# Kernel optimization log

Hardware: AMD Instinct MI355X
Metric: run time of the kernel (lower is better)

Reference implementation:

```python
import jax, jax.numpy as jnp
import numpy as np
from jax import lax

H = 512
V = 32000
B = 64
S = 64
T = 32
TQ = 32
NUM_HOP = 3


def _p(key, shape, scale=0.05):
    return jax.random.normal(key, shape, dtype=jnp.float32) * scale


def setup_inputs() -> dict:
    key = jax.random.key(0)
    ks = jax.random.split(key, 20)
    inp = {}
    inp["contexts"] = jax.random.randint(ks[0], (B, S, T), 0, V)
    inp["questions"] = jax.random.randint(ks[1], (B, TQ), 0, V)
    inp["emb"] = _p(ks[2], (V, H), 1.0)
    # input module: bidirectional GRU (torch gate order r,z,n)
    inp["Wih_f"] = _p(ks[3], (3 * H, H)); inp["Whh_f"] = _p(ks[4], (3 * H, H))
    inp["bih_f"] = jnp.zeros((3 * H,), jnp.float32); inp["bhh_f"] = jnp.zeros((3 * H,), jnp.float32)
    inp["Wih_b"] = _p(ks[5], (3 * H, H)); inp["Whh_b"] = _p(ks[6], (3 * H, H))
    inp["bih_b"] = jnp.zeros((3 * H,), jnp.float32); inp["bhh_b"] = jnp.zeros((3 * H,), jnp.float32)
    # question module GRU
    inp["qWih"] = _p(ks[7], (3 * H, H)); inp["qWhh"] = _p(ks[8], (3 * H, H))
    inp["qbih"] = jnp.zeros((3 * H,), jnp.float32); inp["qbhh"] = jnp.zeros((3 * H,), jnp.float32)
    # attention GRU cell (note: source reuses br as both biases)
    inp["Wr"] = _p(ks[9], (H, H)); inp["Ur"] = _p(ks[10], (H, H)); inp["br"] = jnp.ones((H,), jnp.float32)
    inp["W"] = _p(ks[11], (H, H)); inp["U"] = _p(ks[12], (H, H))
    # episodic memory gate MLP + next-memory projection
    inp["z1_w"] = _p(ks[13], (H, 4 * H)); inp["z1_b"] = jnp.zeros((H,), jnp.float32)
    inp["z2_w"] = _p(ks[14], (1, H)); inp["z2_b"] = jnp.zeros((1,), jnp.float32)
    inp["nm_w"] = _p(ks[15], (H, 3 * H)); inp["nm_b"] = jnp.zeros((H,), jnp.float32)
    # answer module
    inp["ans_w"] = _p(ks[16], (V, 2 * H)); inp["ans_b"] = jnp.zeros((V,), jnp.float32)
    return inp


def _pos_enc(slen, elen):
    # l[s, e] = 1 - s/slen - (e/elen)*(1 - 2*s/slen); indexed by SENTENCE dim, as in source
    s = np.arange(slen, dtype=np.float64)[:, None]
    e = np.arange(elen, dtype=np.float64)[None, :]
    l = 1.0 - s / slen - (e / elen) * (1.0 - 2.0 * s / slen)
    return jnp.asarray(l, dtype=jnp.float32)  # (S, H)


def _gru(x, Wih, Whh, bih, bhh, reverse=False):
    # x: (B, T, H); torch nn.GRU math with gate order r, z, n
    Bn, Tn, Hn = x.shape
    h0 = jnp.zeros((Bn, Hn), x.dtype)

    def step(h, xt):
        gx = xt @ Wih.T + bih
        gh = h @ Whh.T + bhh
        xr, xz, xn = jnp.split(gx, 3, axis=-1)
        hr, hz, hn = jnp.split(gh, 3, axis=-1)
        r = jax.nn.sigmoid(xr + hr)
        z = jax.nn.sigmoid(xz + hz)
        n = jnp.tanh(xn + r * hn)
        h_new = (1.0 - z) * n + z * h
        return h_new, h_new

    h_last, hs = lax.scan(step, h0, jnp.swapaxes(x, 0, 1), reverse=reverse)
    return jnp.swapaxes(hs, 0, 1), h_last


def _dmn(emb, Wih_f, Whh_f, bih_f, bhh_f, Wih_b, Whh_b, bih_b, bhh_b,
         qWih, qWhh, qbih, qbhh, Wr, Ur, br, W, U,
         z1_w, z1_b, z2_w, z2_b, nm_w, nm_b, ans_w, ans_b,
         contexts, questions):
    emb0 = emb.at[0].set(0.0)  # padding_idx=0
    Bn, Sn, Tn = contexts.shape
    Hn = emb.shape[1]
    # ---- input module ----
    ce = emb0[contexts]                                   # (B,S,T,H)
    pe = _pos_enc(Sn, Hn)                                 # (S,H), broadcast over tokens (faithful)
    facts_in = jnp.sum(ce * pe[None, :, None, :], axis=2)  # (B,S,H)
    hf, _ = _gru(facts_in, Wih_f, Whh_f, bih_f, bhh_f, reverse=False)
    hb, _ = _gru(facts_in, Wih_b, Whh_b, bih_b, bhh_b, reverse=True)
    facts = hf + hb                                       # (B,S,H); dropout = identity (eval)
    # ---- question module ----
    _, q = _gru(emb0[questions], qWih, qWhh, qbih, qbhh)  # (B,H)
    # ---- episodic memory hops ----
    facts_t = jnp.swapaxes(facts, 0, 1)                   # (S,B,H)
    M = q
    for _ in range(NUM_HOP):
        qb = q[:, None, :]
        Mb = M[:, None, :]
        z = jnp.concatenate([facts * qb, facts * Mb,
                             jnp.abs(facts - qb), jnp.abs(facts - Mb)], axis=-1)  # (B,S,4H)
        g1 = jnp.tanh(z @ z1_w.T + z1_b)
        G = jax.nn.softmax((g1 @ z2_w.T + z2_b)[..., 0], axis=1)  # (B,S)

        def agru(c, sg):
            fact, g = sg
            r = jax.nn.sigmoid(fact @ Wr + c @ Ur + br)
            ht = jnp.tanh(fact @ W + r * (c @ U) + br)  # source reuses br as b
            return g[:, None] * ht + (1.0 - g[:, None]) * c, None

        C, _ = lax.scan(agru, jnp.zeros((Bn, Hn), facts.dtype), (facts_t, G.T))
        M = jax.nn.relu(jnp.concatenate([M, C, q], axis=-1) @ nm_w.T + nm_b)
    # ---- answer module (dropout = identity) ----
    preds = jnp.concatenate([M, q], axis=-1) @ ans_w.T + ans_b  # (B,V)
    return preds


def reference(contexts, questions, emb, Wih_f, Whh_f, bih_f, bhh_f,
              Wih_b, Whh_b, bih_b, bhh_b, qWih, qWhh, qbih, qbhh,
              Wr, Ur, br, W, U, z1_w, z1_b, z2_w, z2_b, nm_w, nm_b,
              ans_w, ans_b):
    return _dmn(emb, Wih_f, Whh_f, bih_f, bhh_f, Wih_b, Whh_b, bih_b, bhh_b,
                qWih, qWhh, qbih, qbhh, Wr, Ur, br, W, U,
                z1_w, z1_b, z2_w, z2_b, nm_w, nm_b, ans_w, ans_b,
                contexts, questions)
```

## Files before the change

### kernel.cpp

```cpp
#include <hip/hip_runtime.h>
#include <cstddef>
#include <cstdint>

namespace {

constexpr int H  = 512;
constexpr int V  = 32000;
constexpr int B  = 64;
constexpr int S  = 64;
constexpr int T  = 32;
constexpr int TQ = 32;

typedef unsigned short ushort_t;
typedef __attribute__((ext_vector_type(8))) short bf16x8;
typedef __attribute__((ext_vector_type(4))) short bf16x4;
typedef __attribute__((ext_vector_type(4))) float f32x4;
typedef __attribute__((ext_vector_type(4))) unsigned u32x4;

__device__ __forceinline__ ushort_t f2bf(float f) {
  union { float f; unsigned u; } v; v.f = f;
  return (ushort_t)((v.u + 0x7FFFu + ((v.u >> 16) & 1u)) >> 16);
}

__device__ __forceinline__ float sigm(float x) { return 1.f / (1.f + expf(-x)); }

__device__ __forceinline__ bf16x8 pack8(f32x4 a, f32x4 b) {
  bf16x8 r;
  r[0] = (short)f2bf(a[0]); r[1] = (short)f2bf(a[1]);
  r[2] = (short)f2bf(a[2]); r[3] = (short)f2bf(a[3]);
  r[4] = (short)f2bf(b[0]); r[5] = (short)f2bf(b[1]);
  r[6] = (short)f2bf(b[2]); r[7] = (short)f2bf(b[3]);
  return r;
}

__device__ __forceinline__ u32x4 load16c(const void* p) {
  u32x4 v;
  asm volatile("global_load_dwordx4 %0, %1, off sc0 sc1" : "=v"(v) : "v"(p));
  return v;
}
__device__ __forceinline__ void store2c(ushort_t* p, unsigned v) {
  asm volatile("global_store_short %0, %1, off sc0 sc1" :: "v"(p), "v"(v) : "memory");
}
__device__ __forceinline__ void store1cu(unsigned* p, unsigned v) {
  asm volatile("global_store_dword %0, %1, off sc0 sc1" :: "v"(p), "v"(v) : "memory");
}
__device__ __forceinline__ void waitvm0() {
  asm volatile("s_waitcnt vmcnt(0)" ::: "memory");
  __builtin_amdgcn_sched_barrier(0);
}

__device__ __forceinline__ void flag_barrier(unsigned* flags, int rank,
                                             unsigned step1, int t, int lane, int wv) {
  waitvm0();
  __syncthreads();
  if (t == 0) store1cu(flags + rank * 32, step1);
  if (wv == 0) {
    const unsigned* fp = flags + (lane & 7) * 32;
    for (;;) {
      unsigned v;
      asm volatile("global_load_dword %0, %1, off sc0 sc1" : "=v"(v) : "v"(fp));
      asm volatile("s_waitcnt vmcnt(0)" ::: "memory");
      const int ok = (lane >= 8) || (v >= step1);
      if (__all(ok)) break;
      __builtin_amdgcn_s_sleep(1);
    }
  }
  __syncthreads();
}

__global__ __launch_bounds__(256) void k_embed_facts(const int* __restrict__ ctx,
                                                     const float* __restrict__ emb,
                                                     float* __restrict__ facts_in) {
  const int bs = blockIdx.x;
  const int s  = bs & (S - 1);
  const int t  = threadIdx.x;
  __shared__ int sidx[T];
  if (t < T) sidx[t] = ctx[(size_t)bs * T + t];
  __syncthreads();
  float a0 = 0.f, a1 = 0.f;
  for (int tt = 0; tt < T; ++tt) {
    const int ix = sidx[tt];
    if (ix != 0) {
      const float* e = emb + ((size_t)ix << 9);
      a0 += e[t];
      a1 += e[t + 256];
    }
  }
  const float sf = (float)s * (1.f / 64.f);
  const float c1 = 1.f - sf;
  const float c2 = (1.f - 2.f * sf) * (1.f / 512.f);
  facts_in[((size_t)bs << 9) + t]       = a0 * (c1 - (float)t * c2);
  facts_in[((size_t)bs << 9) + t + 256] = a1 * (c1 - (float)(t + 256) * c2);
}

__global__ __launch_bounds__(256) void k_embed_q(const int* __restrict__ qidx,
                                                 const float* __restrict__ emb,
                                                 float* __restrict__ qe) {
  const int bt = blockIdx.x;
  const int t  = threadIdx.x;
  const int ix = qidx[bt];
  float v0 = 0.f, v1 = 0.f;
  if (ix != 0) {
    const float* e = emb + ((size_t)ix << 9);
    v0 = e[t];
    v1 = e[t + 256];
  }
  qe[((size_t)bt << 9) + t]       = v0;
  qe[((size_t)bt << 9) + t + 256] = v1;
}

__global__ __launch_bounds__(256) void k_transpose512(const float* __restrict__ src,
                                                      float* __restrict__ dst) {
  __shared__ float tile[32][33];
  const int x0 = blockIdx.x * 32, y0 = blockIdx.y * 32;
  for (int i = threadIdx.y; i < 32; i += 8)
    tile[i][threadIdx.x] = src[(size_t)(y0 + i) * H + x0 + threadIdx.x];
  __syncthreads();
  for (int i = threadIdx.y; i < 32; i += 8)
    dst[(size_t)(x0 + i) * H + y0 + threadIdx.x] = tile[threadIdx.x][i];
}

template <bool A_BF16, int ACT>
__global__ __launch_bounds__(256) void k_gemm_mfma(const void* __restrict__ Av,
                                                   const float* __restrict__ Bm,
                                                   const float* __restrict__ bias,
                                                   float* __restrict__ C,
                                                   int M, int N, int K) {
  __shared__ __align__(16) ushort_t As[64][72];
  __shared__ __align__(16) ushort_t Bs[64][72];
  const int t    = threadIdx.x;
  const int lane = t & 63;
  const int w    = t >> 6;
  const int wr   = w >> 1, wc = w & 1;
  const int m0 = blockIdx.y << 6, n0 = blockIdx.x << 6;
  const int row = t >> 2;
  const int ch  = t & 3;

  f32x4 acc[2][2] = {};

  for (int k0 = 0; k0 < K; k0 += 64) {
    if (A_BF16) {
      const ushort_t* A16 = (const ushort_t*)Av;
#pragma unroll
      for (int cc = 0; cc < 2; ++cc) {
        const int c8 = ch + cc * 4;
        const uint4 v = *(const uint4*)(A16 + (size_t)(m0 + row) * K + k0 + c8 * 8);
        *(uint4*)&As[row][c8 * 8] = v;
      }
    } else {
      const float* Af = (const float*)Av;
#pragma unroll
      for (int cc = 0; cc < 2; ++cc) {
        const int c8 = ch + cc * 4;
        const float* src = Af + (size_t)(m0 + row) * K + k0 + c8 * 8;
        *(bf16x8*)&As[row][c8 * 8] = pack8(*(const f32x4*)src, *(const f32x4*)(src + 4));
      }
    }
#pragma unroll
    for (int cc = 0; cc < 2; ++cc) {
      const int c8 = ch + cc * 4;
      const float* srb = Bm + (size_t)(n0 + row) * K + k0 + c8 * 8;
      *(bf16x8*)&Bs[row][c8 * 8] = pack8(*(const f32x4*)srb, *(const f32x4*)(srb + 4));
    }
    __syncthreads();
#pragma unroll
    for (int ks = 0; ks < 2; ++ks) {
      bf16x8 a[2], b[2];
#pragma unroll
      for (int fr = 0; fr < 2; ++fr)
        a[fr] = *(const bf16x8*)&As[wr * 32 + fr * 16 + (lane & 15)][ks * 32 + (lane >> 4) * 8];
#pragma unroll
      for (int fc = 0; fc < 2; ++fc)
        b[fc] = *(const bf16x8*)&Bs[wc * 32 + fc * 16 + (lane & 15)][ks * 32 + (lane >> 4) * 8];
#pragma unroll
      for (int fr = 0; fr < 2; ++fr)
#pragma unroll
        for (int fc = 0; fc < 2; ++fc)
          acc[fr][fc] = __builtin_amdgcn_mfma_f32_16x16x32_bf16(a[fr], b[fc], acc[fr][fc], 0, 0, 0);
    }
    __syncthreads();
  }
#pragma unroll
  for (int fr = 0; fr < 2; ++fr) {
#pragma unroll
    for (int fc = 0; fc < 2; ++fc) {
      const int rbase = m0 + wr * 32 + fr * 16 + ((lane >> 4) << 2);
      const int col   = n0 + wc * 32 + fc * 16 + (lane & 15);
      const float bv  = bias ? bias[col] : 0.f;
#pragma unroll
      for (int j = 0; j < 4; ++j) {
        float v = acc[fr][fc][j] + bv;
        if (ACT == 1) v = tanhf(v);
        if (ACT == 2) v = fmaxf(v, 0.f);
        C[(size_t)(rbase + j) * N + col] = v;
      }
    }
  }
}

__global__ __launch_bounds__(256) void k_build_z16(const float* __restrict__ facts,
                                                   const float* __restrict__ q,
                                                   const float* __restrict__ M,
                                                   ushort_t* __restrict__ z) {
  const int bs = blockIdx.x;
  const int b  = bs >> 6;
  const int t  = threadIdx.x;
  const size_t zb = (size_t)bs << 11;
  for (int c = t; c < 512; c += 256) {
    const float f  = facts[((size_t)bs << 9) + c];
    const float qv = q[(b << 9) + c];
    const float mv = M[(b << 9) + c];
    z[zb + c]        = f2bf(f * qv);
    z[zb + 512 + c]  = f2bf(f * mv);
    z[zb + 1024 + c] = f2bf(fabsf(f - qv));
    z[zb + 1536 + c] = f2bf(fabsf(f - mv));
  }
}

__global__ __launch_bounds__(256) void k_gemm_cat3(const float* __restrict__ Mv,
                                                   const float* __restrict__ Cv,
                                                   const float* __restrict__ qv,
                                                   const float* __restrict__ Bm,
                                                   const float* __restrict__ bias,
                                                   float* __restrict__ C) {
  constexpr int N = 512, K = 1536;
  __shared__ __align__(16) ushort_t As[64][72];
  __shared__ __align__(16) ushort_t Bs[64][72];
  const int t    = threadIdx.x;
  const int lane = t & 63;
  const int w    = t >> 6;
  const int wr   = w >> 1, wc = w & 1;
  const int n0 = blockIdx.x << 6;
  const int row = t >> 2;
  const int ch  = t & 3;

  f32x4 acc[2][2] = {};

  for (int k0 = 0; k0 < K; k0 += 64) {
    const int seg = k0 >> 9;
    const float* src = (seg == 0) ? Mv : (seg == 1) ? Cv : qv;
    const int kb = k0 & 511;
#pragma unroll
    for (int cc = 0; cc < 2; ++cc) {
      const int c8 = ch + cc * 4;
      const float* fp = src + ((size_t)row << 9) + kb + c8 * 8;
      *(bf16x8*)&As[row][c8 * 8] = pack8(*(const f32x4*)fp, *(const f32x4*)(fp + 4));
      const float* srb = Bm + (size_t)(n0 + row) * K + k0 + c8 * 8;
      *(bf16x8*)&Bs[row][c8 * 8] = pack8(*(const f32x4*)srb, *(const f32x4*)(srb + 4));
    }
    __syncthreads();
#pragma unroll
    for (int ks = 0; ks < 2; ++ks) {
      bf16x8 a[2], bb[2];
#pragma unroll
      for (int fr = 0; fr < 2; ++fr)
        a[fr] = *(const bf16x8*)&As[wr * 32 + fr * 16 + (lane & 15)][ks * 32 + (lane >> 4) * 8];
#pragma unroll
      for (int fc = 0; fc < 2; ++fc)
        bb[fc] = *(const bf16x8*)&Bs[wc * 32 + fc * 16 + (lane & 15)][ks * 32 + (lane >> 4) * 8];
#pragma unroll
      for (int fr = 0; fr < 2; ++fr)
#pragma unroll
        for (int fc = 0; fc < 2; ++fc)
          acc[fr][fc] = __builtin_amdgcn_mfma_f32_16x16x32_bf16(a[fr], bb[fc], acc[fr][fc], 0, 0, 0);
    }
    __syncthreads();
  }
#pragma unroll
  for (int fr = 0; fr < 2; ++fr) {
#pragma unroll
    for (int fc = 0; fc < 2; ++fc) {
      const int rbase = wr * 32 + fr * 16 + ((lane >> 4) << 2);
      const int col   = n0 + wc * 32 + fc * 16 + (lane & 15);
      const float bv  = bias[col];
#pragma unroll
      for (int j = 0; j < 4; ++j)
        C[(size_t)(rbase + j) * N + col] = fmaxf(acc[fr][fc][j] + bv, 0.f);
    }
  }
}

__global__ __launch_bounds__(256) void k_gemm_cat2(const float* __restrict__ Mv,
                                                   const float* __restrict__ qv,
                                                   const float* __restrict__ Bm,
                                                   const float* __restrict__ bias,
                                                   float* __restrict__ C) {
  constexpr int N = 32000, K = 1024;
  __shared__ __align__(16) ushort_t As[64][72];
  __shared__ __align__(16) ushort_t Bs[64][72];
  const int t    = threadIdx.x;
  const int lane = t & 63;
  const int w    = t >> 6;
  const int wr   = w >> 1, wc = w & 1;
  const int n0 = blockIdx.x << 6;
  const int row = t >> 2;
  const int ch  = t & 3;

  f32x4 acc[2][2] = {};

  for (int k0 = 0; k0 < K; k0 += 64) {
    const float* src = (k0 < 512) ? Mv : qv;
    const int kb = k0 & 511;
#pragma unroll
    for (int cc = 0; cc < 2; ++cc) {
      const int c8 = ch + cc * 4;
      const float* fp = src + ((size_t)row << 9) + kb + c8 * 8;
      *(bf16x8*)&As[row][c8 * 8] = pack8(*(const f32x4*)fp, *(const f32x4*)(fp + 4));
      const float* srb = Bm + (size_t)(n0 + row) * K + k0 + c8 * 8;
      *(bf16x8*)&Bs[row][c8 * 8] = pack8(*(const f32x4*)srb, *(const f32x4*)(srb + 4));
    }
    __syncthreads();
#pragma unroll
    for (int ks = 0; ks < 2; ++ks) {
      bf16x8 a[2], bb[2];
#pragma unroll
      for (int fr = 0; fr < 2; ++fr)
        a[fr] = *(const bf16x8*)&As[wr * 32 + fr * 16 + (lane & 15)][ks * 32 + (lane >> 4) * 8];
#pragma unroll
      for (int fc = 0; fc < 2; ++fc)
        bb[fc] = *(const bf16x8*)&Bs[wc * 32 + fc * 16 + (lane & 15)][ks * 32 + (lane >> 4) * 8];
#pragma unroll
      for (int fr = 0; fr < 2; ++fr)
#pragma unroll
        for (int fc = 0; fc < 2; ++fc)
          acc[fr][fc] = __builtin_amdgcn_mfma_f32_16x16x32_bf16(a[fr], bb[fc], acc[fr][fc], 0, 0, 0);
    }
    __syncthreads();
  }
#pragma unroll
  for (int fr = 0; fr < 2; ++fr) {
#pragma unroll
    for (int fc = 0; fc < 2; ++fc) {
      const int rbase = wr * 32 + fr * 16 + ((lane >> 4) << 2);
      const int col   = n0 + wc * 32 + fc * 16 + (lane & 15);
      const float bv  = bias[col];
#pragma unroll
      for (int j = 0; j < 4; ++j)
        C[(size_t)(rbase + j) * N + col] = acc[fr][fc][j] + bv;
    }
  }
}

__global__ __launch_bounds__(256, 1) void k_gru_scan_mfma(
    const float* __restrict__ Whh_f, const float* __restrict__ bhh_f,
    const float* __restrict__ Whh_b, const float* __restrict__ bhh_b,
    const float* __restrict__ qWhh,  const float* __restrict__ qbhh,
    const float* __restrict__ gx_f, const float* __restrict__ gx_b,
    const float* __restrict__ gx_q,
    ushort_t* __restrict__ H16, float* __restrict__ qbuf,
    float* __restrict__ facts, float* __restrict__ hb_all,
    unsigned* __restrict__ flags_base) {
  const int bx   = blockIdx.x;
  const int grp  = bx >> 3;
  const int rank = bx & 7;
  const int gru  = grp >> 2;
  const int ib   = grp & 3;

  const float* Whh; const float* bhh; const float* gx;
  float* out_seq; int seqlen, rev;
  if (gru == 0)      { Whh = Whh_f; bhh = bhh_f; gx = gx_f; out_seq = facts;   seqlen = S;  rev = 0; }
  else if (gru == 1) { Whh = Whh_b; bhh = bhh_b; gx = gx_b; out_seq = hb_all;  seqlen = S;  rev = 1; }
  else               { Whh = qWhh;  bhh = qbhh;  gx = gx_q; out_seq = nullptr; seqlen = TQ; rev = 0; }
  ushort_t* Hb0 = H16 + gru * 65536;
  ushort_t* Hb1 = Hb0 + 32768;

  __shared__ __align__(16) ushort_t hl[16 * 520];

  const int t    = threadIdx.x;
  const int lane = t & 63;
  const int wv   = t >> 6;
  const int nt   = (rank << 2) + wv;
  const int lm   = lane & 15;
  const int lk   = lane >> 4;
  const int col  = (nt << 4) + lm;

  bf16x8 wf[3][16];
#pragma unroll
  for (int g = 0; g < 3; ++g) {
    const float* wrow = Whh + ((size_t)(g * 512 + col) << 9) + (lk << 3);
#pragma unroll
    for (int ks = 0; ks < 16; ++ks) {
      const float* p = wrow + ks * 32;
      wf[g][ks] = pack8(*(const f32x4*)p, *(const f32x4*)(p + 4));
    }
  }
  const float bv0 = bhh[col], bv1 = bhh[512 + col], bv2 = bhh[1024 + col];
  unsigned* flags = flags_base + grp * 8 * 32;

  float xr[4], xz[4], xn[4];
  {
    const int xidx = rev ? (seqlen - 1) : 0;
#pragma unroll
    for (int j = 0; j < 4; ++j) {
      const int b = (ib << 4) + (lk << 2) + j;
      const size_t gxrow = ((size_t)b * seqlen + xidx) * 1536;
      xr[j] = gx[gxrow + col];
      xz[j] = gx[gxrow + 512 + col];
      xn[j] = gx[gxrow + 1024 + col];
    }
  }

  float hp[4] = {0.f, 0.f, 0.f, 0.f};

  for (int s = 0; s < seqlen; ++s) {
    if (s == 0) {
      for (int i = t; i < 4160; i += 256) ((unsigned*)hl)[i] = 0u;
    } else {
      const ushort_t* Hp16 = (s & 1) ? Hb1 : Hb0;
      u32x4 v[4];
#pragma unroll
      for (int u = 0; u < 4; ++u) {
        const int i = (u << 8) + t;
        v[u] = load16c(Hp16 + ((size_t)((ib << 4) + (i >> 6)) << 9) + ((i << 3) & 511));
      }
      waitvm0();
#pragma unroll
      for (int u = 0; u < 4; ++u) {
        const int i = (u << 8) + t;
        *(u32x4*)&hl[(i >> 6) * 520 + ((i << 3) & 511)] = v[u];
      }
    }
    __syncthreads();

    f32x4 acc0 = {}, acc1 = {}, acc2 = {};
#pragma unroll
    for (int ks = 0; ks < 16; ++ks) {
      const bf16x8 a = *(const bf16x8*)&hl[lm * 520 + (ks << 5) + (lk << 3)];
      acc0 = __builtin_amdgcn_mfma_f32_16x16x32_bf16(a, wf[0][ks], acc0, 0, 0, 0);
      acc1 = __builtin_amdgcn_mfma_f32_16x16x32_bf16(a, wf[1][ks], acc1, 0, 0, 0);
      acc2 = __builtin_amdgcn_mfma_f32_16x16x32_bf16(a, wf[2][ks], acc2, 0, 0, 0);
    }

    const int xidx = rev ? (seqlen - 1 - s) : s;
    ushort_t* Hn16 = (s & 1) ? Hb0 : Hb1;
#pragma unroll
    for (int j = 0; j < 4; ++j) {
      const int b = (ib << 4) + (lk << 2) + j;
      const float r = sigm(xr[j] + acc0[j] + bv0);
      const float z = sigm(xz[j] + acc1[j] + bv1);
      const float n = tanhf(xn[j] + r * (acc2[j] + bv2));
      const float hnew = (1.f - z) * n + z * hp[j];
      hp[j] = hnew;
      if (s + 1 < seqlen) store2c(Hn16 + ((size_t)b << 9) + col, (unsigned)f2bf(hnew));
      if (out_seq) out_seq[((size_t)(b * S + xidx) << 9) + col] = hnew;
      if (gru == 2 && s == seqlen - 1) qbuf[((size_t)b << 9) + col] = hnew;
    }

    if (s + 1 < seqlen) {
      const int xidx2 = rev ? (seqlen - 2 - s) : (s + 1);
      float nxr[4], nxz[4], nxn[4];
#pragma unroll
      for (int j = 0; j < 4; ++j) {
        const int b = (ib << 4) + (lk << 2) + j;
        const size_t gxrow = ((size_t)b * seqlen + xidx2) * 1536;
        nxr[j] = gx[gxrow + col];
        nxz[j] = gx[gxrow + 512 + col];
        nxn[j] = gx[gxrow + 1024 + col];
      }
      flag_barrier(flags, rank, (unsigned)(s + 1), t, lane, wv);
#pragma unroll
      for (int j = 0; j < 4; ++j) { xr[j] = nxr[j]; xz[j] = nxz[j]; xn[j] = nxn[j]; }
    }
  }
}

__global__ __launch_bounds__(256, 1) void k_agru_scan_mfma(
    const float* __restrict__ UrT, const float* __restrict__ UT,
    const float* __restrict__ fRW, const float* __restrict__ fW,
    const float* __restrict__ br, const float* __restrict__ G,
    ushort_t* __restrict__ C16, float* __restrict__ C0f,
    unsigned* __restrict__ flags_base) {
  const int bx   = blockIdx.x;
  const int grp  = bx >> 3;
  const int rank = bx & 7;
  ushort_t* Cb0 = C16;
  ushort_t* Cb1 = C16 + 32768;

  __shared__ __align__(16) ushort_t cl[16 * 520];

  const int t    = threadIdx.x;
  const int lane = t & 63;
  const int wv   = t >> 6;
  const int nt   = (rank << 2) + wv;
  const int lm   = lane & 15;
  const int lk   = lane >> 4;
  const int col  = (nt << 4) + lm;

  bf16x8 wfr[16], wfu[16];
  {
    const float* r0 = UrT + ((size_t)col << 9) + (lk << 3);
    const float* r1 = UT  + ((size_t)col << 9) + (lk << 3);
#pragma unroll
    for (int ks = 0; ks < 16; ++ks) {
      wfr[ks] = pack8(*(const f32x4*)(r0 + ks * 32), *(const f32x4*)(r0 + ks * 32 + 4));
      wfu[ks] = pack8(*(const f32x4*)(r1 + ks * 32), *(const f32x4*)(r1 + ks * 32 + 4));
    }
  }
  const float brv = br[col];
  unsigned* flags = flags_base + grp * 8 * 32;

  float fr[4], fw[4], gg[4];
#pragma unroll
  for (int j = 0; j < 4; ++j) {
    const int b = (grp << 4) + (lk << 2) + j;
    const size_t fi = ((size_t)(b * S) << 9) + col;
    fr[j] = fRW[fi];
    fw[j] = fW[fi];
    gg[j] = G[b << 6];
  }

  float cp[4] = {0.f, 0.f, 0.f, 0.f};

  for (int s = 0; s < S; ++s) {
    if (s == 0) {
      for (int i = t; i < 4160; i += 256) ((unsigned*)cl)[i] = 0u;
    } else {
      const ushort_t* Cp16 = (s & 1) ? Cb1 : Cb0;
      u32x4 v[4];
#pragma unroll
      for (int u = 0; u < 4; ++u) {
        const int i = (u << 8) + t;
        v[u] = load16c(Cp16 + ((size_t)((grp << 4) + (i >> 6)) << 9) + ((i << 3) & 511));
      }
      waitvm0();
#pragma unroll
      for (int u = 0; u < 4; ++u) {
        const int i = (u << 8) + t;
        *(u32x4*)&cl[(i >> 6) * 520 + ((i << 3) & 511)] = v[u];
      }
    }
    __syncthreads();

    f32x4 accr = {}, accu = {};
#pragma unroll
    for (int ks = 0; ks < 16; ++ks) {
      const bf16x8 a = *(const bf16x8*)&cl[lm * 520 + (ks << 5) + (lk << 3)];
      accr = __builtin_amdgcn_mfma_f32_16x16x32_bf16(a, wfr[ks], accr, 0, 0, 0);
      accu = __builtin_amdgcn_mfma_f32_16x16x32_bf16(a, wfu[ks], accu, 0, 0, 0);
    }

    ushort_t* Cn16 = (s & 1) ? Cb0 : Cb1;
#pragma unroll
    for (int j = 0; j < 4; ++j) {
      const int b = (grp << 4) + (lk << 2) + j;
      const float r  = sigm(fr[j] + accr[j] + brv);
      const float ht = tanhf(fw[j] + r * accu[j] + brv);
      const float cnew = gg[j] * ht + (1.f - gg[j]) * cp[j];
      cp[j] = cnew;
      if (s + 1 < S) store2c(Cn16 + ((size_t)b << 9) + col, (unsigned)f2bf(cnew));
      else           C0f[((size_t)b << 9) + col] = cnew;
    }

    if (s + 1 < S) {
      float nfr[4], nfw[4], ngg[4];
#pragma unroll
      for (int j = 0; j < 4; ++j) {
        const int b = (grp << 4) + (lk << 2) + j;
        const size_t fi = ((size_t)(b * S + s + 1) << 9) + col;
        nfr[j] = fRW[fi];
        nfw[j] = fW[fi];
        ngg[j] = G[(b << 6) + s + 1];
      }
      flag_barrier(flags, rank, (unsigned)(s + 1), t, lane, wv);
#pragma unroll
      for (int j = 0; j < 4; ++j) { fr[j] = nfr[j]; fw[j] = nfw[j]; gg[j] = ngg[j]; }
    }
  }
}

__global__ __launch_bounds__(256) void k_add(float* __restrict__ a, const float* __restrict__ b) {
  const size_t i = (((size_t)blockIdx.x << 8) + threadIdx.x) << 2;
  float4 x = *(float4*)(a + i);
  const float4 y = *(const float4*)(b + i);
  x.x += y.x; x.y += y.y; x.z += y.z; x.w += y.w;
  *(float4*)(a + i) = x;
}

__global__ __launch_bounds__(256) void k_score_softmax(const float* __restrict__ g1,
                                                       const float* __restrict__ z2w,
                                                       const float* __restrict__ z2b,
                                                       float* __restrict__ G) {
  const int b = blockIdx.x, t = threadIdx.x;
  const int wave = t >> 6, lane = t & 63;
  __shared__ float sc[64];
  for (int si = 0; si < 16; ++si) {
    const int s = wave * 16 + si;
    const float* row = g1 + ((size_t)(b * S + s) << 9) + lane * 8;
    const float* w   = z2w + lane * 8;
    float p = 0.f;
#pragma unroll
    for (int k = 0; k < 8; ++k) p += row[k] * w[k];
#pragma unroll
    for (int off = 32; off; off >>= 1) p += __shfl_xor(p, off);
    if (lane == 0) sc[s] = p + z2b[0];
  }
  __syncthreads();
  if (wave == 0) {
    const float v = sc[lane];
    float m = v;
#pragma unroll
    for (int off = 32; off; off >>= 1) m = fmaxf(m, __shfl_xor(m, off));
    const float e = expf(v - m);
    float su = e;
#pragma unroll
    for (int off = 32; off; off >>= 1) su += __shfl_xor(su, off);
    G[(b << 6) + lane] = e / su;
  }
}

}

extern "C" void kernel_launch(void* const* d_in, const int* in_sizes, int n_in,
                              void* d_out, int out_size, void* d_ws, size_t ws_size,
                              hipStream_t stream) {
  const int*   contexts  = (const int*)d_in[0];
  const int*   questions = (const int*)d_in[1];
  const float* emb   = (const float*)d_in[2];
  const float* Wih_f = (const float*)d_in[3];
  const float* Whh_f = (const float*)d_in[4];
  const float* bih_f = (const float*)d_in[5];
  const float* bhh_f = (const float*)d_in[6];
  const float* Wih_b = (const float*)d_in[7];
  const float* Whh_b = (const float*)d_in[8];
  const float* bih_b = (const float*)d_in[9];
  const float* bhh_b = (const float*)d_in[10];
  const float* qWih  = (const float*)d_in[11];
  const float* qWhh  = (const float*)d_in[12];
  const float* qbih  = (const float*)d_in[13];
  const float* qbhh  = (const float*)d_in[14];
  const float* Wr    = (const float*)d_in[15];
  const float* Ur    = (const float*)d_in[16];
  const float* br    = (const float*)d_in[17];
  const float* Wm    = (const float*)d_in[18];
  const float* Um    = (const float*)d_in[19];
  const float* z1_w  = (const float*)d_in[20];
  const float* z1_b  = (const float*)d_in[21];
  const float* z2_w  = (const float*)d_in[22];
  const float* z2_b  = (const float*)d_in[23];
  const float* nm_w  = (const float*)d_in[24];
  const float* nm_b  = (const float*)d_in[25];
  const float* ans_w = (const float*)d_in[26];
  const float* ans_b = (const float*)d_in[27];
  (void)in_sizes; (void)n_in; (void)out_size; (void)ws_size;

  float* ws = (float*)d_ws;
  float* WrT      = ws + 0;
  float* UrT      = ws + 262144;
  float* WT       = ws + 524288;
  float* UT       = ws + 786432;
  float* facts_in = ws + 1048576;
  float* qe       = ws + 3145728;
  float* gx_f     = ws + 4194304;
  float* gx_b     = ws + 10485760;
  float* gx_q     = ws + 16777216;
  float* facts    = ws + 19922944;
  float* hb       = ws + 22020096;
  float* Hbuf     = ws + 24117248;
  float* C0       = ws + 24313856;
  float* M0       = ws + 24379392;
  float* M1       = ws + 24412160;
  float* Mq       = ws + 24543232;
  float* Gm       = ws + 24608768;
  ushort_t* H16 = (ushort_t*)Hbuf;
  float* qbuf   = Hbuf + 98304;
  ushort_t* C16 = (ushort_t*)(Hbuf + 131072);
  ushort_t* zb16 = (ushort_t*)gx_f;
  float* g1  = gx_q;
  float* fRW = facts_in;
  float* fW  = hb;
  float* preds = (float*)d_out;
  unsigned* bar = (unsigned*)Mq;
  float* q = qbuf;

  hipMemsetAsync(bar, 0, 6144 * sizeof(unsigned), stream);

  k_embed_facts<<<B * S, 256, 0, stream>>>(contexts, emb, facts_in);
  k_embed_q<<<B * TQ, 256, 0, stream>>>(questions, emb, qe);
  dim3 tb(32, 8);
  k_transpose512<<<dim3(16, 16), tb, 0, stream>>>(Wr, WrT);
  k_transpose512<<<dim3(16, 16), tb, 0, stream>>>(Ur, UrT);
  k_transpose512<<<dim3(16, 16), tb, 0, stream>>>(Wm, WT);
  k_transpose512<<<dim3(16, 16), tb, 0, stream>>>(Um, UT);

  k_gemm_mfma<false, 0><<<dim3(24, 64), 256, 0, stream>>>(facts_in, Wih_f, bih_f, gx_f, 4096, 1536, 512);
  k_gemm_mfma<false, 0><<<dim3(24, 64), 256, 0, stream>>>(facts_in, Wih_b, bih_b, gx_b, 4096, 1536, 512);
  k_gemm_mfma<false, 0><<<dim3(24, 32), 256, 0, stream>>>(qe, qWih, qbih, gx_q, 2048, 1536, 512);

  k_gru_scan_mfma<<<96, 256, 0, stream>>>(Whh_f, bhh_f, Whh_b, bhh_b, qWhh, qbhh,
                                          gx_f, gx_b, gx_q, H16, qbuf, facts, hb, bar);
  k_add<<<2048, 256, 0, stream>>>(facts, hb);

  k_gemm_mfma<false, 0><<<dim3(8, 64), 256, 0, stream>>>(facts, WrT, nullptr, fRW, 4096, 512, 512);
  k_gemm_mfma<false, 0><<<dim3(8, 64), 256, 0, stream>>>(facts, WT,  nullptr, fW,  4096, 512, 512);

  const float* Mcur = q;
  for (int h = 0; h < 3; ++h) {
    k_build_z16<<<B * S, 256, 0, stream>>>(facts, q, Mcur, zb16);
    k_gemm_mfma<true, 1><<<dim3(8, 64), 256, 0, stream>>>(zb16, z1_w, z1_b, g1, 4096, 512, 2048);
    k_score_softmax<<<B, 256, 0, stream>>>(g1, z2_w, z2_b, Gm);
    unsigned* fl = bar + 3072 + h * 1024;
    k_agru_scan_mfma<<<32, 256, 0, stream>>>(UrT, UT, fRW, fW, br, Gm, C16, C0, fl);
    float* Mnext = (h & 1) ? M1 : M0;
    k_gemm_cat3<<<dim3(8, 1), 256, 0, stream>>>(Mcur, C0, q, nm_w, nm_b, Mnext);
    Mcur = Mnext;
  }

  k_gemm_cat2<<<dim3(500, 1), 256, 0, stream>>>(Mcur, q, ans_w, ans_b, preds);
}
```

Measured before the change: 1.400 ms.

## Replace flag barriers in GRU scans with step-tagged hidden-state words

The GRU and attention-GRU scan kernels previously used a per-step cross-block flag barrier before reading the shared hidden state. Now each hidden value is stored as a 32-bit word holding the bf16 value and a step tag, and consumers poll until each chunk carries the expected tag. This drops the global barrier round trip and lets blocks proceed as soon as their data arrives. The cost is doubled hidden-state traffic, per-chunk polling loops, and the loss of next-step input prefetching that the old barrier code overlapped.

```diff
diff --git a/kernel.cpp b/kernel.cpp
--- a/kernel.cpp
+++ b/kernel.cpp
@@ -33,39 +33,17 @@
   return r;
 }
 
-__device__ __forceinline__ u32x4 load16c(const void* p) {
+__device__ __forceinline__ u32x4 ld16c(const unsigned* p) {
   u32x4 v;
   asm volatile("global_load_dwordx4 %0, %1, off sc0 sc1" : "=v"(v) : "v"(p));
   return v;
 }
-__device__ __forceinline__ void store2c(ushort_t* p, unsigned v) {
-  asm volatile("global_store_short %0, %1, off sc0 sc1" :: "v"(p), "v"(v) : "memory");
-}
-__device__ __forceinline__ void store1cu(unsigned* p, unsigned v) {
+__device__ __forceinline__ void st4c(unsigned* p, unsigned v) {
   asm volatile("global_store_dword %0, %1, off sc0 sc1" :: "v"(p), "v"(v) : "memory");
 }
 __device__ __forceinline__ void waitvm0() {
   asm volatile("s_waitcnt vmcnt(0)" ::: "memory");
   __builtin_amdgcn_sched_barrier(0);
-}
-
-__device__ __forceinline__ void flag_barrier(unsigned* flags, int rank,
-                                             unsigned step1, int t, int lane, int wv) {
-  waitvm0();
-  __syncthreads();
-  if (t == 0) store1cu(flags + rank * 32, step1);
-  if (wv == 0) {
-    const unsigned* fp = flags + (lane & 7) * 32;
-    for (;;) {
-      unsigned v;
-      asm volatile("global_load_dword %0, %1, off sc0 sc1" : "=v"(v) : "v"(fp));
-      asm volatile("s_waitcnt vmcnt(0)" ::: "memory");
-      const int ok = (lane >= 8) || (v >= step1);
-      if (__all(ok)) break;
-      __builtin_amdgcn_s_sleep(1);
-    }
-  }
-  __syncthreads();
 }
 
 __global__ __launch_bounds__(256) void k_embed_facts(const int* __restrict__ ctx,
@@ -341,15 +319,52 @@
   }
 }
 
+__device__ __forceinline__ void stage_tagged(const unsigned* __restrict__ buf,
+                                             unsigned want, int rows0, int t,
+                                             ushort_t* __restrict__ lds) {
+  const int item = t >> 4;
+  const int colb = (t & 15) << 5;
+  const unsigned* base = buf + ((size_t)(rows0 + item) << 9) + colb;
+  u32x4 q0, q1, q2, q3, q4, q5, q6, q7;
+  unsigned pend = 0xFFu;
+  for (;;) {
+    if (pend & 0x01u) q0 = ld16c(base + 0);
+    if (pend & 0x02u) q1 = ld16c(base + 4);
+    if (pend & 0x04u) q2 = ld16c(base + 8);
+    if (pend & 0x08u) q3 = ld16c(base + 12);
+    if (pend & 0x10u) q4 = ld16c(base + 16);
+    if (pend & 0x20u) q5 = ld16c(base + 20);
+    if (pend & 0x40u) q6 = ld16c(base + 24);
+    if (pend & 0x80u) q7 = ld16c(base + 28);
+    waitvm0();
+    unsigned np = 0;
+#define CHK(qq, bit, off)                                                       \
+    if (pend & bit) {                                                           \
+      if (((qq[0] & 0xFFFFu) == want) && ((qq[1] & 0xFFFFu) == want) &&         \
+          ((qq[2] & 0xFFFFu) == want) && ((qq[3] & 0xFFFFu) == want)) {         \
+        bf16x4 r;                                                               \
+        r[0] = (short)(qq[0] >> 16); r[1] = (short)(qq[1] >> 16);               \
+        r[2] = (short)(qq[2] >> 16); r[3] = (short)(qq[3] >> 16);               \
+        *(bf16x4*)&lds[item * 520 + colb + off] = r;                            \
+      } else np |= bit;                                                         \
+    }
+    CHK(q0, 0x01u, 0)  CHK(q1, 0x02u, 4)  CHK(q2, 0x04u, 8)  CHK(q3, 0x08u, 12)
+    CHK(q4, 0x10u, 16) CHK(q5, 0x20u, 20) CHK(q6, 0x40u, 24) CHK(q7, 0x80u, 28)
+#undef CHK
+    pend = np;
+    if (!pend) break;
+    __builtin_amdgcn_s_sleep(4);
+  }
+}
+
 __global__ __launch_bounds__(256, 1) void k_gru_scan_mfma(
     const float* __restrict__ Whh_f, const float* __restrict__ bhh_f,
     const float* __restrict__ Whh_b, const float* __restrict__ bhh_b,
     const float* __restrict__ qWhh,  const float* __restrict__ qbhh,
     const float* __restrict__ gx_f, const float* __restrict__ gx_b,
     const float* __restrict__ gx_q,
-    ushort_t* __restrict__ H16, float* __restrict__ qbuf,
-    float* __restrict__ facts, float* __restrict__ hb_all,
-    unsigned* __restrict__ flags_base) {
+    unsigned* __restrict__ Hg, float* __restrict__ qbuf,
+    float* __restrict__ facts, float* __restrict__ hb_all) {
   const int bx   = blockIdx.x;
   const int grp  = bx >> 3;
   const int rank = bx & 7;
@@ -361,8 +376,8 @@
   if (gru == 0)      { Whh = Whh_f; bhh = bhh_f; gx = gx_f; out_seq = facts;   seqlen = S;  rev = 0; }
   else if (gru == 1) { Whh = Whh_b; bhh = bhh_b; gx = gx_b; out_seq = hb_all;  seqlen = S;  rev = 1; }
   else               { Whh = qWhh;  bhh = qbhh;  gx = gx_q; out_seq = nullptr; seqlen = TQ; rev = 0; }
-  ushort_t* Hb0 = H16 + gru * 65536;
-  ushort_t* Hb1 = Hb0 + 32768;
+  unsigned* Hg0 = Hg + gru * 65536;
+  unsigned* Hg1 = Hg0 + 32768;
 
   __shared__ __align__(16) ushort_t hl[16 * 520];
 
@@ -385,11 +400,12 @@
     }
   }
   const float bv0 = bhh[col], bv1 = bhh[512 + col], bv2 = bhh[1024 + col];
-  unsigned* flags = flags_base + grp * 8 * 32;
-
-  float xr[4], xz[4], xn[4];
-  {
-    const int xidx = rev ? (seqlen - 1) : 0;
+
+  float hp[4] = {0.f, 0.f, 0.f, 0.f};
+
+  for (int s = 0; s < seqlen; ++s) {
+    const int xidx = rev ? (seqlen - 1 - s) : s;
+    float xr[4], xz[4], xn[4];
 #pragma unroll
     for (int j = 0; j < 4; ++j) {
       const int b = (ib << 4) + (lk << 2) + j;
@@ -398,27 +414,12 @@
       xz[j] = gx[gxrow + 512 + col];
       xn[j] = gx[gxrow + 1024 + col];
     }
-  }
-
-  float hp[4] = {0.f, 0.f, 0.f, 0.f};
-
-  for (int s = 0; s < seqlen; ++s) {
+
     if (s == 0) {
       for (int i = t; i < 4160; i += 256) ((unsigned*)hl)[i] = 0u;
     } else {
-      const ushort_t* Hp16 = (s & 1) ? Hb1 : Hb0;
-      u32x4 v[4];
-#pragma unroll
-      for (int u = 0; u < 4; ++u) {
-        const int i = (u << 8) + t;
-        v[u] = load16c(Hp16 + ((size_t)((ib << 4) + (i >> 6)) << 9) + ((i << 3) & 511));
-      }
-      waitvm0();
-#pragma unroll
-      for (int u = 0; u < 4; ++u) {
-        const int i = (u << 8) + t;
-        *(u32x4*)&hl[(i >> 6) * 520 + ((i << 3) & 511)] = v[u];
-      }
+      const unsigned* Hp = (s & 1) ? Hg1 : Hg0;
+      stage_tagged(Hp, (unsigned)s, ib << 4, t, hl);
     }
     __syncthreads();
 
@@ -431,8 +432,7 @@
       acc2 = __builtin_amdgcn_mfma_f32_16x16x32_bf16(a, wf[2][ks], acc2, 0, 0, 0);
     }
 
-    const int xidx = rev ? (seqlen - 1 - s) : s;
-    ushort_t* Hn16 = (s & 1) ? Hb0 : Hb1;
+    unsigned* Hn = (s & 1) ? Hg0 : Hg1;
 #pragma unroll
     for (int j = 0; j < 4; ++j) {
       const int b = (ib << 4) + (lk << 2) + j;
@@ -441,26 +441,13 @@
       const float n = tanhf(xn[j] + r * (acc2[j] + bv2));
       const float hnew = (1.f - z) * n + z * hp[j];
       hp[j] = hnew;
-      if (s + 1 < seqlen) store2c(Hn16 + ((size_t)b << 9) + col, (unsigned)f2bf(hnew));
+      if (s + 1 < seqlen)
+        st4c(Hn + ((size_t)b << 9) + col,
+             ((unsigned)f2bf(hnew) << 16) | (unsigned)(s + 1));
       if (out_seq) out_seq[((size_t)(b * S + xidx) << 9) + col] = hnew;
       if (gru == 2 && s == seqlen - 1) qbuf[((size_t)b << 9) + col] = hnew;
     }
-
-    if (s + 1 < seqlen) {
-      const int xidx2 = rev ? (seqlen - 2 - s) : (s + 1);
-      float nxr[4], nxz[4], nxn[4];
-#pragma unroll
-      for (int j = 0; j < 4; ++j) {
-        const int b = (ib << 4) + (lk << 2) + j;
-        const size_t gxrow = ((size_t)b * seqlen + xidx2) * 1536;
-        nxr[j] = gx[gxrow + col];
-        nxz[j] = gx[gxrow + 512 + col];
-        nxn[j] = gx[gxrow + 1024 + col];
-      }
-      flag_barrier(flags, rank, (unsigned)(s + 1), t, lane, wv);
-#pragma unroll
-      for (int j = 0; j < 4; ++j) { xr[j] = nxr[j]; xz[j] = nxz[j]; xn[j] = nxn[j]; }
-    }
+    __syncthreads();
   }
 }
 
@@ -468,13 +455,12 @@
     const float* __restrict__ UrT, const float* __restrict__ UT,
     const float* __restrict__ fRW, const float* __restrict__ fW,
     const float* __restrict__ br, const float* __restrict__ G,
-    ushort_t* __restrict__ C16, float* __restrict__ C0f,
-    unsigned* __restrict__ flags_base) {
+    unsigned* __restrict__ Ct, float* __restrict__ C0f, int tagbase) {
   const int bx   = blockIdx.x;
   const int grp  = bx >> 3;
   const int rank = bx & 7;
-  ushort_t* Cb0 = C16;
-  ushort_t* Cb1 = C16 + 32768;
+  unsigned* Ct0 = Ct;
+  unsigned* Ct1 = Ct + 32768;
 
   __shared__ __align__(16) ushort_t cl[16 * 520];
 
@@ -497,37 +483,25 @@
     }
   }
   const float brv = br[col];
-  unsigned* flags = flags_base + grp * 8 * 32;
-
-  float fr[4], fw[4], gg[4];
-#pragma unroll
-  for (int j = 0; j < 4; ++j) {
-    const int b = (grp << 4) + (lk << 2) + j;
-    const size_t fi = ((size_t)(b * S) << 9) + col;
-    fr[j] = fRW[fi];
-    fw[j] = fW[fi];
-    gg[j] = G[b << 6];
-  }
 
   float cp[4] = {0.f, 0.f, 0.f, 0.f};
 
   for (int s = 0; s < S; ++s) {
+    float fr[4], fw[4], gg[4];
+#pragma unroll
+    for (int j = 0; j < 4; ++j) {
+      const int b = (grp << 4) + (lk << 2) + j;
+      const size_t fi = ((size_t)(b * S + s) << 9) + col;
+      fr[j] = fRW[fi];
+      fw[j] = fW[fi];
+      gg[j] = G[(b << 6) + s];
+    }
+
     if (s == 0) {
       for (int i = t; i < 4160; i += 256) ((unsigned*)cl)[i] = 0u;
     } else {
-      const ushort_t* Cp16 = (s & 1) ? Cb1 : Cb0;
-      u32x4 v[4];
-#pragma unroll
-      for (int u = 0; u < 4; ++u) {
-        const int i = (u << 8) + t;
-        v[u] = load16c(Cp16 + ((size_t)((grp << 4) + (i >> 6)) << 9) + ((i << 3) & 511));
-      }
-      waitvm0();
-#pragma unroll
-      for (int u = 0; u < 4; ++u) {
-        const int i = (u << 8) + t;
-        *(u32x4*)&cl[(i >> 6) * 520 + ((i << 3) & 511)] = v[u];
-      }
+      const unsigned* Cp = (s & 1) ? Ct1 : Ct0;
+      stage_tagged(Cp, (unsigned)(tagbase + s), grp << 4, t, cl);
     }
     __syncthreads();
 
@@ -539,7 +513,7 @@
       accu = __builtin_amdgcn_mfma_f32_16x16x32_bf16(a, wfu[ks], accu, 0, 0, 0);
     }
 
-    ushort_t* Cn16 = (s & 1) ? Cb0 : Cb1;
+    unsigned* Cn = (s & 1) ? Ct0 : Ct1;
 #pragma unroll
     for (int j = 0; j < 4; ++j) {
       const int b = (grp << 4) + (lk << 2) + j;
@@ -547,24 +521,13 @@
       const float ht = tanhf(fw[j] + r * accu[j] + brv);
       const float cnew = gg[j] * ht + (1.f - gg[j]) * cp[j];
       cp[j] = cnew;
-      if (s + 1 < S) store2c(Cn16 + ((size_t)b << 9) + col, (unsigned)f2bf(cnew));
-      else           C0f[((size_t)b << 9) + col] = cnew;
-    }
-
-    if (s + 1 < S) {
-      float nfr[4], nfw[4], ngg[4];
-#pragma unroll
-      for (int j = 0; j < 4; ++j) {
-        const int b = (grp << 4) + (lk << 2) + j;
-        const size_t fi = ((size_t)(b * S + s + 1) << 9) + col;
-        nfr[j] = fRW[fi];
-        nfw[j] = fW[fi];
-        ngg[j] = G[(b << 6) + s + 1];
-      }
-      flag_barrier(flags, rank, (unsigned)(s + 1), t, lane, wv);
-#pragma unroll
-      for (int j = 0; j < 4; ++j) { fr[j] = nfr[j]; fw[j] = nfw[j]; gg[j] = ngg[j]; }
-    }
+      if (s + 1 < S)
+        st4c(Cn + ((size_t)b << 9) + col,
+             ((unsigned)f2bf(cnew) << 16) | (unsigned)(tagbase + s + 1));
+      else
+        C0f[((size_t)b << 9) + col] = cnew;
+    }
+    __syncthreads();
   }
 }
 
@@ -655,24 +618,21 @@
   float* gx_q     = ws + 16777216;
   float* facts    = ws + 19922944;
   float* hb       = ws + 22020096;
-  float* Hbuf     = ws + 24117248;
-  float* C0       = ws + 24313856;
-  float* M0       = ws + 24379392;
-  float* M1       = ws + 24412160;
-  float* Mq       = ws + 24543232;
-  float* Gm       = ws + 24608768;
-  ushort_t* H16 = (ushort_t*)Hbuf;
-  float* qbuf   = Hbuf + 98304;
-  ushort_t* C16 = (ushort_t*)(Hbuf + 131072);
+  unsigned* Hg = (unsigned*)(ws + 24117248);
+  unsigned* Ct = (unsigned*)(ws + 24313856);
+  float* C0   = ws + 24379392;
+  float* qbuf = ws + 24412160;
+  float* M0   = ws + 24444928;
+  float* M1   = ws + 24477696;
+  float* Gm   = ws + 24510464;
   ushort_t* zb16 = (ushort_t*)gx_f;
   float* g1  = gx_q;
   float* fRW = facts_in;
   float* fW  = hb;
   float* preds = (float*)d_out;
-  unsigned* bar = (unsigned*)Mq;
   float* q = qbuf;
 
-  hipMemsetAsync(bar, 0, 6144 * sizeof(unsigned), stream);
+  hipMemsetAsync(Hg, 0, (196608 + 65536) * sizeof(unsigned), stream);
 
   k_embed_facts<<<B * S, 256, 0, stream>>>(contexts, emb, facts_in);
   k_embed_q<<<B * TQ, 256, 0, stream>>>(questions, emb, qe);
@@ -687,7 +647,7 @@
   k_gemm_mfma<false, 0><<<dim3(24, 32), 256, 0, stream>>>(qe, qWih, qbih, gx_q, 2048, 1536, 512);
 
   k_gru_scan_mfma<<<96, 256, 0, stream>>>(Whh_f, bhh_f, Whh_b, bhh_b, qWhh, qbhh,
-                                          gx_f, gx_b, gx_q, H16, qbuf, facts, hb, bar);
+                                          gx_f, gx_b, gx_q, Hg, qbuf, facts, hb);
   k_add<<<2048, 256, 0, stream>>>(facts, hb);
 
   k_gemm_mfma<false, 0><<<dim3(8, 64), 256, 0, stream>>>(facts, WrT, nullptr, fRW, 4096, 512, 512);
@@ -698,8 +658,7 @@
     k_build_z16<<<B * S, 256, 0, stream>>>(facts, q, Mcur, zb16);
     k_gemm_mfma<true, 1><<<dim3(8, 64), 256, 0, stream>>>(zb16, z1_w, z1_b, g1, 4096, 512, 2048);
     k_score_softmax<<<B, 256, 0, stream>>>(g1, z2_w, z2_b, Gm);
-    unsigned* fl = bar + 3072 + h * 1024;
-    k_agru_scan_mfma<<<32, 256, 0, stream>>>(UrT, UT, fRW, fW, br, Gm, C16, C0, fl);
+    k_agru_scan_mfma<<<32, 256, 0, stream>>>(UrT, UT, fRW, fW, br, Gm, Ct, C0, h * 64);
     float* Mnext = (h & 1) ? M1 : M0;
     k_gemm_cat3<<<dim3(8, 1), 256, 0, stream>>>(Mcur, C0, q, nm_w, nm_b, Mnext);
     Mcur = Mnext;
```

Result: slower. 1.524 ms (+8.9%).
